# Optimization experiments

Measured on AMD Instinct MI355X. Metric: run time of the kernel, lower is better.

## Reference

```python
import jax, jax.numpy as jnp
import numpy as np

N = 262144          # total points
C = 16              # classes
AVG_DEG = 16
E = N * AVG_DEG     # edges
LAMBDA1 = 0.7
LAMBDA2 = 0.5
LAMBDA_S = 0.2
LOSS_WEIGHT = 1.0
IGNORE_INDEX = -1
EPS = 1e-8


def setup_inputs() -> dict:
    key = jax.random.key(0)
    k1, k2, k3, k4 = jax.random.split(key, 4)
    pred = jax.random.normal(k1, (N, C), dtype=jnp.float32)
    target = jax.random.randint(k2, (N,), 0, C, dtype=jnp.int64)
    # precomputed radius-graph edge list (row = destination, col = source)
    row = jax.random.randint(k3, (E,), 0, N, dtype=jnp.int64)
    col = jax.random.randint(k4, (E,), 0, N, dtype=jnp.int64)
    return {"pred": pred, "target": target, "row": row, "col": col}


def _masked_mean(x, mask):
    cnt = jnp.sum(mask.astype(x.dtype))
    s = jnp.sum(jnp.where(mask, x, jnp.zeros_like(x)))
    return jnp.where(cnt > 0, s / jnp.maximum(cnt, 1.0), s)


def reference(pred, target, row, col):
    # per-point CE (reduction='none'); ignored points contribute 0
    log_probs = jax.nn.log_softmax(pred, axis=1)          # [N, C]
    probs = jnp.exp(log_probs)                            # [N, C]
    valid_mask = target != IGNORE_INDEX
    tgt = jnp.where(valid_mask, target, 0)
    ce_per_point = -jnp.take_along_axis(log_probs, tgt[:, None], axis=1)[:, 0]
    ce_per_point = jnp.where(valid_mask, ce_per_point, 0.0)

    conf = jnp.max(probs, axis=1)                         # [N]
    pred_label = jnp.argmax(probs, axis=1)                # [N]

    # degree per destination node
    deg = jax.ops.segment_sum(jnp.ones((E,), dtype=probs.dtype), row, num_segments=N)

    # neighborhood agreement u_i = mean_{j in N(i)} [pred_j == pred_i]
    agree_edge = (pred_label[col] == pred_label[row]).astype(probs.dtype)
    sum_agree = jax.ops.segment_sum(agree_edge, row, num_segments=N)
    u = jnp.where(deg > 0, sum_agree / jnp.maximum(deg, 1.0), jnp.ones_like(sum_agree))

    w = 1.0 + LAMBDA1 * (1.0 - u) + LAMBDA2 * (1.0 - conf)
    loss_ce = _masked_mean(w * ce_per_point, valid_mask)

    # per-edge KL(p_i || p_j) with clamp at 1e-8, scatter-mean over neighbors
    pi = probs[row]                                       # [E, C]
    pj = probs[col]                                       # [E, C]
    kl_edge = jnp.sum(
        pi * (jnp.log(jnp.maximum(pi, EPS)) - jnp.log(jnp.maximum(pj, EPS))), axis=1
    )                                                     # [E]
    sum_kl = jax.ops.segment_sum(kl_edge, row, num_segments=N)
    mean_kl = jnp.where(deg > 0, sum_kl / jnp.maximum(deg, 1.0), jnp.zeros_like(sum_kl))
    loss_smooth = _masked_mean(mean_kl, valid_mask)

    return (loss_ce + LAMBDA_S * loss_smooth) * LOSS_WEIGHT
```

## Files before the change

### kernel.cpp

```cpp
#include <hip/hip_runtime.h>

constexpr float LAMBDA1  = 0.7f;
constexpr float LAMBDA2  = 0.5f;
constexpr float LAMBDA_S = 0.2f;
constexpr float LOG_EPS  = -18.420680743952367f;
constexpr float PQ_SCALE  = 15.0f;
constexpr float LQ_SCALE4 = 15.0f / 18.420680743952367f;
constexpr float DOT_SCALE4 = 18.420680743952367f / (15.0f * 15.0f);

constexpr int      BUCK_SHIFT = 10;
constexpr unsigned BUCK_CAP   = 20480u;
constexpr int      CHUNK      = 8192;
constexpr int      FT         = 1024;
constexpr int      EPT        = CHUNK / FT;
constexpr int      RT         = 1024;
constexpr int      CUR_PAD    = 16;
constexpr int      BPW        = 256 / (FT / 64);

#if defined(__has_builtin)
#if __has_builtin(__builtin_amdgcn_udot8)
#define HAS_UDOT8 1
#endif
#endif

__global__ void __launch_bounds__(FT, 8)
k_fused(const float* __restrict__ pred,
        const int*   __restrict__ target,
        unsigned long long* __restrict__ probsQ4,
        unsigned long long* __restrict__ logpQ4,
        float* __restrict__ Hn,
        float* __restrict__ confn,
        float* __restrict__ cen,
        const int* __restrict__ row,
        const int* __restrict__ col,
        unsigned* __restrict__ bucketed,
        unsigned* __restrict__ gcursor,
        int n, int e, int bucketBlocks) {
    int t = threadIdx.x;

    if ((int)blockIdx.x < bucketBlocks) {
        __shared__ unsigned stage[CHUNK];
        __shared__ unsigned hist[256];
        __shared__ unsigned cnt[256];
        __shared__ unsigned lofs[256];
        __shared__ unsigned baseArr[256];

        if (t < 256) { hist[t] = 0; cnt[t] = 0; }
        __syncthreads();

        long i0 = (long)blockIdx.x * CHUNK;
        int chunkN = (int)(((long)e - i0) < CHUNK ? ((long)e - i0) : CHUNK);
        if (chunkN < 0) chunkN = 0;

        int rr[EPT], cc[EPT];
#pragma unroll
        for (int j = 0; j < EPT; ++j) {
            int k = t + j * FT;
            if (k < chunkN) {
                rr[j] = __builtin_nontemporal_load(row + i0 + k);
                cc[j] = __builtin_nontemporal_load(col + i0 + k);
                atomicAdd(&hist[rr[j] >> BUCK_SHIFT], 1u);
            }
        }
        __syncthreads();

        if (t < 64) {
            unsigned h0 = hist[4 * t], h1 = hist[4 * t + 1],
                     h2 = hist[4 * t + 2], h3 = hist[4 * t + 3];
            unsigned s = h0 + h1 + h2 + h3;
            unsigned inc = s;
#pragma unroll
            for (int off = 1; off < 64; off <<= 1) {
                unsigned v = __shfl_up(inc, off, 64);
                if (t >= off) inc += v;
            }
            unsigned run = inc - s;
            lofs[4 * t]     = run;
            lofs[4 * t + 1] = run + h0;
            lofs[4 * t + 2] = run + h0 + h1;
            lofs[4 * t + 3] = run + h0 + h1 + h2;
#pragma unroll
            for (int j = 0; j < 4; ++j) {
                int b = 4 * t + j;
                unsigned h = hist[b];
                baseArr[b] = (unsigned)b * BUCK_CAP
                           + atomicAdd(&gcursor[b * CUR_PAD], h);
            }
        }
        __syncthreads();

#pragma unroll
        for (int j = 0; j < EPT; ++j) {
            int k = t + j * FT;
            if (k < chunkN) {
                int b = rr[j] >> BUCK_SHIFT;
                unsigned s = lofs[b] + atomicAdd(&cnt[b], 1u);
                stage[s] = ((unsigned)(rr[j] & 1023) << 18) | (unsigned)cc[j];
            }
        }
        __syncthreads();

        {
            int wave = t >> 6, lane = t & 63;
#pragma unroll
            for (int j = 0; j < BPW; ++j) {
                int b = wave * BPW + j;
                unsigned cb    = hist[b];
                unsigned lo    = lofs[b];
                unsigned gbase = baseArr[b];
                unsigned lim   = (unsigned)(b + 1) * BUCK_CAP;
                unsigned m = (gbase >= lim) ? 0u
                           : (cb < lim - gbase ? cb : lim - gbase);
                for (unsigned i = lane; i < m; i += 64)
                    bucketed[gbase + i] = stage[lo + i];
            }
        }
    } else {
        int i = (blockIdx.x - bucketBlocks) * FT + t;
        if (i >= n) return;

        const float4* p4 = reinterpret_cast<const float4*>(pred + (size_t)i * 16);
        float4 v0 = p4[0], v1 = p4[1], v2 = p4[2], v3 = p4[3];
        float x[16] = {v0.x, v0.y, v0.z, v0.w,
                       v1.x, v1.y, v1.z, v1.w,
                       v2.x, v2.y, v2.z, v2.w,
                       v3.x, v3.y, v3.z, v3.w};

        float m = x[0];
#pragma unroll
        for (int c = 1; c < 16; ++c) m = fmaxf(m, x[c]);

        float s = 0.f;
#pragma unroll
        for (int c = 0; c < 16; ++c) s += __expf(x[c] - m);
        float logZ = m + __logf(s);

        unsigned long long pq64 = 0ull, lq64 = 0ull;
        float Hacc = 0.f;
#pragma unroll
        for (int c = 0; c < 16; ++c) {
            float lp  = x[c] - logZ;
            float p   = __expf(lp);
            float lpc = fmaxf(lp, LOG_EPS);
            Hacc += p * lpc;

            unsigned pq = (unsigned)(int)rintf(p * PQ_SCALE);
            unsigned lq = (unsigned)(int)rintf(-lpc * LQ_SCALE4);
            pq64 |= (unsigned long long)pq << (4 * c);
            lq64 |= (unsigned long long)lq << (4 * c);
        }

        probsQ4[i] = pq64;
        logpQ4[i]  = lq64;

        Hn[i]    = Hacc;
        confn[i] = __expf(m - logZ);

        int tt0 = target[i];
        bool valid = (tt0 != -1);
        int tt = valid ? tt0 : 0;
        float xt = x[0];
#pragma unroll
        for (int c = 1; c < 16; ++c) xt = (c == tt) ? x[c] : xt;
        cen[i] = valid ? -(xt - logZ) : 0.f;
    }
}

__global__ void __launch_bounds__(RT)
k_reduce(const unsigned* __restrict__ bucketed,
         const unsigned* __restrict__ gcursor,
         const unsigned long long* __restrict__ probsQ4,
         const unsigned long long* __restrict__ logpQ4,
         const int*   __restrict__ target,
         const float* __restrict__ confn,
         const float* __restrict__ cen,
         const float* __restrict__ Hn,
         float* __restrict__ partial,
         int n) {
    __shared__ unsigned long long acc[1024];
    __shared__ unsigned long long Ptab[1024];
    __shared__ unsigned char labr[1024];
    __shared__ float sred[3][16];
    int t = threadIdx.x;
    int b = blockIdx.x;

    {
        acc[t] = 0ull;
        int node = (b << BUCK_SHIFT) + t;
        unsigned long long P = (node < n)
            ? __builtin_nontemporal_load(probsQ4 + node) : 0ull;
        Ptab[t] = P;
        unsigned plo = (unsigned)P, phi = (unsigned)(P >> 32);
        int lr = 0, mr = -1;
#pragma unroll
        for (int k2 = 0; k2 < 8; ++k2) {
            int pv = (int)((plo >> (4 * k2)) & 15u);
            if (pv > mr) { mr = pv; lr = k2; }
        }
#pragma unroll
        for (int k2 = 0; k2 < 8; ++k2) {
            int pv = (int)((phi >> (4 * k2)) & 15u);
            if (pv > mr) { mr = pv; lr = 8 + k2; }
        }
        labr[t] = (unsigned char)lr;
    }
    __syncthreads();

    unsigned nb = gcursor[b * CUR_PAD];
    if (nb > BUCK_CAP) nb = BUCK_CAP;
    unsigned base = (unsigned)b * BUCK_CAP;

    for (unsigned k = (unsigned)t; k < nb; k += RT) {
        unsigned pl = __builtin_nontemporal_load(bucketed + base + k);
        unsigned c  = pl & 0x3FFFFu;
        unsigned lr = pl >> 18;
        unsigned long long P = Ptab[lr];
        unsigned long long L = logpQ4[c];
        unsigned plo = (unsigned)P, phi = (unsigned)(P >> 32);
        unsigned llo = (unsigned)L, lhi = (unsigned)(L >> 32);

        unsigned dot;
#ifdef HAS_UDOT8
        dot = __builtin_amdgcn_udot8(plo, llo, 0u, false);
        dot = __builtin_amdgcn_udot8(phi, lhi, dot, false);
#else
        dot = 0;
#pragma unroll
        for (int k2 = 0; k2 < 8; ++k2) {
            dot += ((plo >> (4 * k2)) & 15u) * ((llo >> (4 * k2)) & 15u);
            dot += ((phi >> (4 * k2)) & 15u) * ((lhi >> (4 * k2)) & 15u);
        }
#endif
        int lab_c = 0, mc = 1000;
#pragma unroll
        for (int k2 = 0; k2 < 8; ++k2) {
            int lv = (int)((llo >> (4 * k2)) & 15u);
            if (lv < mc) { mc = lv; lab_c = k2; }
        }
#pragma unroll
        for (int k2 = 0; k2 < 8; ++k2) {
            int lv = (int)((lhi >> (4 * k2)) & 15u);
            if (lv < mc) { mc = lv; lab_c = 8 + k2; }
        }

        unsigned agree = ((int)labr[lr] == lab_c) ? 1u : 0u;
        unsigned long long add =
            ((unsigned long long)(0x10000u | agree) << 32)
            | (unsigned long long)dot;
        atomicAdd(&acc[lr], add);
    }
    __syncthreads();

    float wce = 0.f, mkl = 0.f, v = 0.f;
    {
        int node = (b << BUCK_SHIFT) + t;
        if (node < n) {
            unsigned long long pk = acc[t];
            float deg  = (float)(unsigned)(pk >> 48);
            float sag  = (float)(unsigned)((pk >> 32) & 0xFFFFu);
            float sdot = (float)(unsigned)(pk & 0xFFFFFFFFull);
            float u  = (deg > 0.f) ? sag / deg : 1.f;
            float hn = __builtin_nontemporal_load(Hn + node);
            float cf = __builtin_nontemporal_load(confn + node);
            float ce = __builtin_nontemporal_load(cen + node);
            int   tg = __builtin_nontemporal_load(target + node);
            float mk = (deg > 0.f) ? (hn + sdot * DOT_SCALE4 / deg) : 0.f;
            float w  = 1.f + LAMBDA1 * (1.f - u) + LAMBDA2 * (1.f - cf);
            if (tg != -1) {
                wce = w * ce;
                mkl = mk;
                v   = 1.f;
            }
        }
    }
#pragma unroll
    for (int off = 32; off > 0; off >>= 1) {
        wce += __shfl_down(wce, off, 64);
        mkl += __shfl_down(mkl, off, 64);
        v   += __shfl_down(v,   off, 64);
    }
    int wave = t >> 6, lane = t & 63;
    if (lane == 0) { sred[0][wave] = wce; sred[1][wave] = mkl; sred[2][wave] = v; }
    __syncthreads();
    if (t < 16) {
        float a = sred[0][t], bb = sred[1][t], c = sred[2][t];
#pragma unroll
        for (int off = 8; off > 0; off >>= 1) {
            a  += __shfl_down(a,  off, 64);
            bb += __shfl_down(bb, off, 64);
            c  += __shfl_down(c,  off, 64);
        }
        if (t == 0) {
            float4* p4 = reinterpret_cast<float4*>(partial);
            p4[b] = make_float4(a, bb, c, 0.f);
        }
    }
}

__global__ void k_final(const float* __restrict__ partial, float* __restrict__ out) {
    int t = threadIdx.x;
    const float4* p4 = reinterpret_cast<const float4*>(partial);
    float4 pv = p4[t];
    float wce = pv.x, mkl = pv.y, v = pv.z;
#pragma unroll
    for (int off = 32; off > 0; off >>= 1) {
        wce += __shfl_down(wce, off, 64);
        mkl += __shfl_down(mkl, off, 64);
        v   += __shfl_down(v,   off, 64);
    }
    __shared__ float s[3][4];
    int wave = t >> 6, lane = t & 63;
    if (lane == 0) { s[0][wave] = wce; s[1][wave] = mkl; s[2][wave] = v; }
    __syncthreads();
    if (t == 0) {
        float a = 0.f, b = 0.f, c = 0.f;
#pragma unroll
        for (int w = 0; w < 4; ++w) { a += s[0][w]; b += s[1][w]; c += s[2][w]; }
        float lce = (c > 0.f) ? a / fmaxf(c, 1.f) : a;
        float ls  = (c > 0.f) ? b / fmaxf(c, 1.f) : b;
        out[0] = lce + LAMBDA_S * ls;
    }
}

extern "C" void kernel_launch(void* const* d_in, const int* in_sizes, int n_in,
                              void* d_out, int out_size, void* d_ws, size_t ws_size,
                              hipStream_t stream) {
    const float* pred   = (const float*)d_in[0];
    const int*   target = (const int*)d_in[1];
    const int*   row    = (const int*)d_in[2];
    const int*   col    = (const int*)d_in[3];
    float* out = (float*)d_out;

    const int n = in_sizes[1];
    const int e = in_sizes[2];

    const int nbuck = (n + 1023) >> BUCK_SHIFT;
    const int bucketBlocks = (e + CHUNK - 1) / CHUNK;
    const int pointBlocks  = (n + FT - 1) / FT;

    char* base = (char*)d_ws;
    size_t off = 0;
    unsigned long long* probsQ4 = (unsigned long long*)(base + off); off += (size_t)n * 8;
    unsigned long long* logpQ4  = (unsigned long long*)(base + off); off += (size_t)n * 8;
    float* Hn     = (float*)(base + off); off += (size_t)n * sizeof(float);
    float* confn  = (float*)(base + off); off += (size_t)n * sizeof(float);
    float* cen    = (float*)(base + off); off += (size_t)n * sizeof(float);
    unsigned* bucketed = (unsigned*)(base + off); off += (size_t)nbuck * BUCK_CAP * 4;
    unsigned* gcursor  = (unsigned*)(base + off); off += (size_t)nbuck * CUR_PAD * 4;
    float* partial = (float*)(base + off); off += (size_t)nbuck * 4 * sizeof(float);

    hipMemsetAsync(gcursor, 0, (size_t)nbuck * CUR_PAD * 4, stream);

    k_fused<<<bucketBlocks + pointBlocks, FT, 0, stream>>>(
        pred, target, probsQ4, logpQ4, Hn, confn, cen,
        row, col, bucketed, gcursor, n, e, bucketBlocks);
    k_reduce<<<nbuck, RT, 0, stream>>>(bucketed, gcursor, probsQ4, logpQ4,
                                       target, confn, cen, Hn, partial, n);
    k_final<<<1, 256, 0, stream>>>(partial, out);
}
```

Measured before the change: 134.5 us.

## Double bucketing chunk size and overlap global cursor atomics with LDS scatter

Doubles the edge chunk handled per bucketing block, halving the number of blocks and the per-bucket global cursor atomics. Packed payloads and 8-bit bucket ids are kept in registers so twice as many edges fit. The global cursor atomics are moved past the barrier so their latency overlaps the shared-memory scatter into the stage buffer. The stage buffer doubles to 64 KB and register use rises, which may lower occupancy.

```diff
diff --git a/kernel.cpp b/kernel.cpp
--- a/kernel.cpp
+++ b/kernel.cpp
@@ -10,7 +10,7 @@
 
 constexpr int      BUCK_SHIFT = 10;
 constexpr unsigned BUCK_CAP   = 20480u;
-constexpr int      CHUNK      = 8192;
+constexpr int      CHUNK      = 16384;
 constexpr int      FT         = 1024;
 constexpr int      EPT        = CHUNK / FT;
 constexpr int      RT         = 1024;
@@ -52,15 +52,22 @@
         int chunkN = (int)(((long)e - i0) < CHUNK ? ((long)e - i0) : CHUNK);
         if (chunkN < 0) chunkN = 0;
 
-        int rr[EPT], cc[EPT];
+        unsigned pay[EPT];
+        unsigned bidp[EPT / 4];
 #pragma unroll
         for (int j = 0; j < EPT; ++j) {
             int k = t + j * FT;
+            unsigned b = 0u, p = 0u;
             if (k < chunkN) {
-                rr[j] = __builtin_nontemporal_load(row + i0 + k);
-                cc[j] = __builtin_nontemporal_load(col + i0 + k);
-                atomicAdd(&hist[rr[j] >> BUCK_SHIFT], 1u);
-            }
+                int r = __builtin_nontemporal_load(row + i0 + k);
+                int c = __builtin_nontemporal_load(col + i0 + k);
+                b = (unsigned)r >> BUCK_SHIFT;
+                p = ((unsigned)(r & 1023) << 18) | (unsigned)c;
+                atomicAdd(&hist[b], 1u);
+            }
+            if ((j & 3) == 0) bidp[j >> 2] = (b & 255u);
+            else              bidp[j >> 2] |= (b & 255u) << (8 * (j & 3));
+            pay[j] = p;
         }
         __syncthreads();
 
@@ -79,24 +86,31 @@
             lofs[4 * t + 1] = run + h0;
             lofs[4 * t + 2] = run + h0 + h1;
             lofs[4 * t + 3] = run + h0 + h1 + h2;
+        }
+        __syncthreads();
+
+        unsigned myBase[4];
+        if (t < 64) {
 #pragma unroll
             for (int j = 0; j < 4; ++j) {
                 int b = 4 * t + j;
-                unsigned h = hist[b];
-                baseArr[b] = (unsigned)b * BUCK_CAP
-                           + atomicAdd(&gcursor[b * CUR_PAD], h);
-            }
-        }
-        __syncthreads();
+                myBase[j] = (unsigned)b * BUCK_CAP
+                          + atomicAdd(&gcursor[b * CUR_PAD], hist[b]);
+            }
+        }
 
 #pragma unroll
         for (int j = 0; j < EPT; ++j) {
             int k = t + j * FT;
             if (k < chunkN) {
-                int b = rr[j] >> BUCK_SHIFT;
+                unsigned b = (bidp[j >> 2] >> (8 * (j & 3))) & 255u;
                 unsigned s = lofs[b] + atomicAdd(&cnt[b], 1u);
-                stage[s] = ((unsigned)(rr[j] & 1023) << 18) | (unsigned)cc[j];
-            }
+                stage[s] = pay[j];
+            }
+        }
+        if (t < 64) {
+#pragma unroll
+            for (int j = 0; j < 4; ++j) baseArr[4 * t + j] = myBase[j];
         }
         __syncthreads();
 
```

Result: faster. 129.7 us (-3.6%).
